# Optimization experiments

Hardware: AMD Instinct MI355X
Metric: run time of the kernel (lower is better)

## Reference

```python
import jax, jax.numpy as jnp
import numpy as np


def _bilinear_resize(x, out_h, out_w):
    """PyTorch F.interpolate(mode='bilinear', align_corners=False) on NCHW."""
    H, W = x.shape[-2], x.shape[-1]

    def coords(out, inp):
        scale = inp / out
        src = (jnp.arange(out, dtype=jnp.float32) + 0.5) * scale - 0.5
        src = jnp.clip(src, 0.0, inp - 1)
        lo = jnp.floor(src).astype(jnp.int32)
        hi = jnp.minimum(lo + 1, inp - 1)
        w = src - lo.astype(jnp.float32)
        return lo, hi, w

    yl, yh, wy = coords(out_h, H)
    xl, xh, wx = coords(out_w, W)
    rows = x[..., yl, :] * (1.0 - wy)[:, None] + x[..., yh, :] * wy[:, None]  # (B,F,out_h,W)
    out = rows[..., xl] * (1.0 - wx) + rows[..., xh] * wx  # (B,F,out_h,out_w)
    return out


def setup_inputs() -> dict:
    key = jax.random.key(0)
    x = jax.random.normal(key, (32, 3, 256, 256), dtype=jnp.float32)
    return {"x": x}


def reference(x):
    B, C, H, W = x.shape
    feats = []
    for p in (2, 4, 8):
        stride = p // 2
        n = (H - p) // stride + 1  # square input -> nh == nw == n
        starts = jnp.arange(n) * stride
        off = jnp.arange(p)
        idx = starts[:, None] + off[None, :]  # (n, p)
        # gather overlapping windows: (B,C,n,p,W) -> (B,C,n,p,n,p)
        xp = x[:, :, idx, :]
        xp = xp[:, :, :, :, idx]
        # -> (B,C,n,n,p,p) row-major patch flatten, matching torch unfold
        xp = xp.transpose(0, 1, 2, 4, 3, 5).reshape(B, C, n * n, p * p)
        mean = xp.mean(-1)                               # (B,C,N)
        std = jnp.std(xp, axis=-1, ddof=1) + 1e-6        # unbiased, like torch.std
        if p == 2:
            a, b, c, d = xp[..., 0], xp[..., 1], xp[..., 2], xp[..., 3]
            raw = a * d - b * c                          # det of 2x2 patch
            det = jnp.sign(raw) * jnp.abs(raw) ** 0.7
            det = det.mean(axis=1, keepdims=True)        # (B,1,N)
            comb = jnp.concatenate([mean, std, det], axis=1)
        else:
            comb = jnp.concatenate([mean, std], axis=1)
        spatial = comb.reshape(B, -1, n, n)
        feats.append(_bilinear_resize(spatial, 32, 32))
    return jnp.concatenate(feats, axis=1)  # (B, 19, 32, 32) for C=3
```

## Files before the change

### kernel.cpp

```cpp
#include <hip/hip_runtime.h>
#include <math.h>


__device__ __forceinline__ float hsum4(float4 q) { return q.x + q.y + q.z + q.w; }
__device__ __forceinline__ float hsq4(float4 q) {
    return q.x * q.x + q.y * q.y + q.z * q.z + q.w * q.w;
}

__device__ __forceinline__ float signed_pow07(float raw) {
    float a = fabsf(raw);
    float r = exp2f(0.7f * log2f(fmaxf(a, 1e-38f)));
    return copysignf(r, raw);
}

template <int N>
__device__ __forceinline__ void bilin(int o, int& lo, float& w) {
    const float scale = (float)N / 32.0f;
    float s = (o + 0.5f) * scale - 0.5f;
    s = fminf(fmaxf(s, 0.0f), (float)(N - 1));
    lo = (int)floorf(s);
    w = s - (float)lo;
}

__device__ __forceinline__ void spds_scale8(const float* __restrict__ x,
                                            float* __restrict__ out, int tid) {
    constexpr int N = 63;
    constexpr float INV_PP = 1.0f / 64.0f, INV_PPM1 = 1.0f / 63.0f;

    int lane_y = tid & 1;
    int t      = tid >> 1;
    int ox     = t & 31;
    int oy     = (t >> 5) & 31;
    int u      = t >> 10;
    int b      = u / 3;
    int c      = u - 3 * b;

    int yl, xl; float wy, wx;
    bilin<N>(oy, yl, wy);
    bilin<N>(ox, xl, wx);

    float wly = lane_y ? wy : (1.0f - wy);
    float wl  = (1.0f - wx) * wly;
    float wr  = wx * wly;

    const float* xc = x + ((size_t)b * 3 + c) * 65536 + xl * 4;

    int rb    = yl * 4 + (lane_y ? 11 : 0);
    int rstep = lane_y ? -256 : 256;
    const float* p = xc + rb * 256;
    float Xs_l = 0, Xs_r = 0, Xq_l = 0, Xq_r = 0;
    float Ys_l = 0, Ys_r = 0, Yq_l = 0, Yq_r = 0;
    #pragma unroll
    for (int dy = 0; dy < 6; ++dy) {
        const float4* r = reinterpret_cast<const float4*>(p);
        float4 q0 = r[0], q1 = r[1], q2 = r[2];
        float s0 = hsum4(q0), s1 = hsum4(q1), s2 = hsum4(q2);
        float t0 = hsq4(q0),  t1 = hsq4(q1),  t2 = hsq4(q2);
        float srl = s0 + s1, srr = s1 + s2;
        float trl = t0 + t1, trr = t1 + t2;
        Xs_l += srl; Xs_r += srr; Xq_l += trl; Xq_r += trr;
        if (dy < 4) { Ys_l += srl; Ys_r += srr; Yq_l += trl; Yq_r += trr; }
        p += rstep;
    }
    float Zs_l = Xs_l - Ys_l, Zs_r = Xs_r - Ys_r;
    float Zq_l = Xq_l - Yq_l, Zq_r = Xq_r - Yq_r;
    float sl  = Xs_l + __shfl_xor(Zs_l, 1);
    float sr  = Xs_r + __shfl_xor(Zs_r, 1);
    float ssl = Xq_l + __shfl_xor(Zq_l, 1);
    float ssr = Xq_r + __shfl_xor(Zq_r, 1);

    float ml = sl * INV_PP, mr = sr * INV_PP;
    float vl = (ssl - sl * sl * INV_PP) * INV_PPM1;
    float vr = (ssr - sr * sr * INV_PP) * INV_PPM1;
    float dl = sqrtf(fmaxf(vl, 0.0f)) + 1e-6f;
    float dr = sqrtf(fmaxf(vr, 0.0f)) + 1e-6f;

    float vmean = ml * wl + mr * wr;
    float vstd  = dl * wl + dr * wr;
    vmean += __shfl_xor(vmean, 1);
    vstd  += __shfl_xor(vstd, 1);

    if (lane_y == 0) {
        float* ob = out + ((size_t)b * 19 + 13 + c) * 1024 + oy * 32 + ox;
        ob[0]        = vmean;
        ob[3 * 1024] = vstd;
    }
}

template <int P, int CHBASE>
__device__ __forceinline__ void spds_scale(const float* __restrict__ x,
                                           float* __restrict__ out, int tid) {
    constexpr int N = (256 - P) / (P / 2) + 1;
    constexpr int NV = (P == 2) ? 7 : 6;
    constexpr int PP = P * P;
    constexpr float INV_PP   = 1.0f / PP;
    constexpr float INV_PPM1 = 1.0f / (PP - 1);

    int lane_y = tid & 1;
    int t      = tid >> 1;
    int ox     = t & 31;
    int oy     = (t >> 5) & 31;
    int b      = t >> 10;

    int yl, xl; float wy, wx;
    bilin<N>(oy, yl, wy);
    bilin<N>(ox, xl, wx);

    float wly = lane_y ? wy : (1.0f - wy);
    float wl  = (1.0f - wx) * wly;
    float wr  = wx * wly;

    const float* xb = x + (size_t)b * 3 * 65536 + xl * (P / 2);

    float vals[7];
    float det = 0.0f;

    #pragma unroll
    for (int c = 0; c < 3; ++c) {
        const float* xc = xb + (size_t)c * 65536;
        float sl, ssl, sr, ssr;
        float rawl = 0.0f, rawr = 0.0f;

        if constexpr (P == 4) {
            int rb    = yl * 2 + (lane_y ? 5 : 0);
            int rstep = lane_y ? -256 : 256;
            const float* p = xc + rb * 256;
            float Xs_l = 0, Xs_r = 0, Xq_l = 0, Xq_r = 0;
            float Ys_l = 0, Ys_r = 0, Yq_l = 0, Yq_r = 0;
            #pragma unroll
            for (int dy = 0; dy < 3; ++dy) {
                const float2* r = reinterpret_cast<const float2*>(p);
                float2 u = r[0], v = r[1], w2 = r[2];
                float s0 = u.x + u.y, s1 = v.x + v.y, s2 = w2.x + w2.y;
                float t0 = u.x * u.x + u.y * u.y;
                float t1 = v.x * v.x + v.y * v.y;
                float t2 = w2.x * w2.x + w2.y * w2.y;
                float srl = s0 + s1, srr = s1 + s2;
                float trl = t0 + t1, trr = t1 + t2;
                Xs_l += srl; Xs_r += srr; Xq_l += trl; Xq_r += trr;
                if (dy < 2) { Ys_l += srl; Ys_r += srr; Yq_l += trl; Yq_r += trr; }
                p += rstep;
            }
            float Zs_l = Xs_l - Ys_l, Zs_r = Xs_r - Ys_r;
            float Zq_l = Xq_l - Yq_l, Zq_r = Xq_r - Yq_r;
            sl  = Xs_l + __shfl_xor(Zs_l, 1);
            sr  = Xs_r + __shfl_xor(Zs_r, 1);
            ssl = Xq_l + __shfl_xor(Zq_l, 1);
            ssr = Xq_r + __shfl_xor(Zq_r, 1);
        } else {
            const float* p0 = xc + (yl + lane_y) * 256;
            float a  = p0[0],   b2 = p0[1],   e = p0[2];
            float c2 = p0[256], d  = p0[257], g = p0[258];
            sl  = a + b2 + c2 + d;
            sr  = b2 + e + d + g;
            ssl = a * a + b2 * b2 + c2 * c2 + d * d;
            ssr = b2 * b2 + e * e + d * d + g * g;
            rawl = a * d - b2 * c2;
            rawr = b2 * g - e * d;
        }

        float ml = sl * INV_PP, mr = sr * INV_PP;
        float vl = (ssl - sl * sl * INV_PP) * INV_PPM1;
        float vr = (ssr - sr * sr * INV_PP) * INV_PPM1;
        float dl = sqrtf(fmaxf(vl, 0.0f)) + 1e-6f;
        float dr = sqrtf(fmaxf(vr, 0.0f)) + 1e-6f;

        vals[c]     = ml * wl + mr * wr;
        vals[3 + c] = dl * wl + dr * wr;
        if constexpr (P == 2)
            det += signed_pow07(rawl) * wl + signed_pow07(rawr) * wr;
    }
    if constexpr (P == 2) vals[6] = det * (1.0f / 3.0f);

    #pragma unroll
    for (int i = 0; i < NV; ++i) {
        float v = vals[i];
        v += __shfl_xor(v, 1);
        vals[i] = v;
    }

    if (lane_y == 0) {
        float* ob = out + ((size_t)b * 19 + CHBASE) * 1024 + oy * 32 + ox;
        #pragma unroll
        for (int i = 0; i < NV; ++i)
            ob[(size_t)i * 1024] = vals[i];
    }
}

__global__ __launch_bounds__(256) void spds_fused(const float* __restrict__ x,
                                                  float* __restrict__ out,
                                                  int bps8, int bps) {
    int bid = blockIdx.x;
    if (bid < bps8) {
        spds_scale8(x, out, bid * 256 + threadIdx.x);
    } else if (bid < bps8 + bps) {
        spds_scale<4, 7>(x, out, (bid - bps8) * 256 + threadIdx.x);
    } else {
        spds_scale<2, 0>(x, out, (bid - bps8 - bps) * 256 + threadIdx.x);
    }
}

extern "C" void kernel_launch(void* const* d_in, const int* in_sizes, int n_in,
                              void* d_out, int out_size, void* d_ws, size_t ws_size,
                              hipStream_t stream) {
    const float* x   = (const float*)d_in[0];
    float*       out = (float*)d_out;
    int B = in_sizes[0] / (3 * 256 * 256);
    int bps8 = B * 24;
    int bps  = B * 8;
    spds_fused<<<bps8 + 2 * bps, 256, 0, stream>>>(x, out, bps8, bps);
}
```

Measured before the change: 11.13 us.

## Stage 8x8 patch statistics through shared-memory 2x2 and 4x4 block sums

Replaces the per-thread scale-8 path, which reread overlapping 8x8 windows straight from global memory, with a block-cooperative scheme. Each block loads a 68-row band of one channel once, builds 2x2 sum and sum-of-squares partials in LDS, reduces them to 4x4 partials, and assembles each needed 8x8 window from four 4x4 tiles. This halves the scale-8 block count and cuts redundant global reads. In exchange it adds about 43KB of static shared memory to every block of the fused kernel, including the scale-2 and scale-4 blocks that never use it, which may limit occupancy.

Result: slower. 12.73 us (+14.4%).

```diff
diff --git a/kernel.cpp b/kernel.cpp
--- a/kernel.cpp
+++ b/kernel.cpp
@@ -20,71 +20,6 @@
     s = fminf(fmaxf(s, 0.0f), (float)(N - 1));
     lo = (int)floorf(s);
     w = s - (float)lo;
-}
-
-__device__ __forceinline__ void spds_scale8(const float* __restrict__ x,
-                                            float* __restrict__ out, int tid) {
-    constexpr int N = 63;
-    constexpr float INV_PP = 1.0f / 64.0f, INV_PPM1 = 1.0f / 63.0f;
-
-    int lane_y = tid & 1;
-    int t      = tid >> 1;
-    int ox     = t & 31;
-    int oy     = (t >> 5) & 31;
-    int u      = t >> 10;
-    int b      = u / 3;
-    int c      = u - 3 * b;
-
-    int yl, xl; float wy, wx;
-    bilin<N>(oy, yl, wy);
-    bilin<N>(ox, xl, wx);
-
-    float wly = lane_y ? wy : (1.0f - wy);
-    float wl  = (1.0f - wx) * wly;
-    float wr  = wx * wly;
-
-    const float* xc = x + ((size_t)b * 3 + c) * 65536 + xl * 4;
-
-    int rb    = yl * 4 + (lane_y ? 11 : 0);
-    int rstep = lane_y ? -256 : 256;
-    const float* p = xc + rb * 256;
-    float Xs_l = 0, Xs_r = 0, Xq_l = 0, Xq_r = 0;
-    float Ys_l = 0, Ys_r = 0, Yq_l = 0, Yq_r = 0;
-    #pragma unroll
-    for (int dy = 0; dy < 6; ++dy) {
-        const float4* r = reinterpret_cast<const float4*>(p);
-        float4 q0 = r[0], q1 = r[1], q2 = r[2];
-        float s0 = hsum4(q0), s1 = hsum4(q1), s2 = hsum4(q2);
-        float t0 = hsq4(q0),  t1 = hsq4(q1),  t2 = hsq4(q2);
-        float srl = s0 + s1, srr = s1 + s2;
-        float trl = t0 + t1, trr = t1 + t2;
-        Xs_l += srl; Xs_r += srr; Xq_l += trl; Xq_r += trr;
-        if (dy < 4) { Ys_l += srl; Ys_r += srr; Yq_l += trl; Yq_r += trr; }
-        p += rstep;
-    }
-    float Zs_l = Xs_l - Ys_l, Zs_r = Xs_r - Ys_r;
-    float Zq_l = Xq_l - Yq_l, Zq_r = Xq_r - Yq_r;
-    float sl  = Xs_l + __shfl_xor(Zs_l, 1);
-    float sr  = Xs_r + __shfl_xor(Zs_r, 1);
-    float ssl = Xq_l + __shfl_xor(Zq_l, 1);
-    float ssr = Xq_r + __shfl_xor(Zq_r, 1);
-
-    float ml = sl * INV_PP, mr = sr * INV_PP;
-    float vl = (ssl - sl * sl * INV_PP) * INV_PPM1;
-    float vr = (ssr - sr * sr * INV_PP) * INV_PPM1;
-    float dl = sqrtf(fmaxf(vl, 0.0f)) + 1e-6f;
-    float dr = sqrtf(fmaxf(vr, 0.0f)) + 1e-6f;
-
-    float vmean = ml * wl + mr * wr;
-    float vstd  = dl * wl + dr * wr;
-    vmean += __shfl_xor(vmean, 1);
-    vstd  += __shfl_xor(vstd, 1);
-
-    if (lane_y == 0) {
-        float* ob = out + ((size_t)b * 19 + 13 + c) * 1024 + oy * 32 + ox;
-        ob[0]        = vmean;
-        ob[3 * 1024] = vstd;
-    }
 }
 
 template <int P, int CHBASE>
@@ -189,14 +124,105 @@
 
 __global__ __launch_bounds__(256) void spds_fused(const float* __restrict__ x,
                                                   float* __restrict__ out,
-                                                  int bps8, int bps) {
+                                                  int nb8, int bps) {
+    __shared__ float2 B22[34 * 128];
+    __shared__ float2 B44[17 * 64];
+
     int bid = blockIdx.x;
-    if (bid < bps8) {
-        spds_scale8(x, out, bid * 256 + threadIdx.x);
-    } else if (bid < bps8 + bps) {
-        spds_scale<4, 7>(x, out, (bid - bps8) * 256 + threadIdx.x);
+    if (bid < nb8) {
+        int rem = bid % 12;
+        int b   = bid / 12;
+        int c   = rem >> 2;
+        int t   = rem & 3;
+        const int R0q_tab[4] = {0, 16, 31, 47};
+        int R0q = R0q_tab[t];
+        int R0  = R0q * 4;
+
+        const float* xc = x + ((size_t)b * 3 + c) * 65536;
+
+        #pragma unroll
+        for (int k = 0; k < 9; ++k) {
+            int tau = threadIdx.x + 256 * k;
+            if (tau < 34 * 64) {
+                int q = tau & 63;
+                int r2 = tau >> 6;
+                const float* p = xc + (R0 + 2 * r2) * 256 + 4 * q;
+                float4 a  = *reinterpret_cast<const float4*>(p);
+                float4 b4 = *reinterpret_cast<const float4*>(p + 256);
+                float s0  = a.x + a.y + b4.x + b4.y;
+                float ss0 = a.x * a.x + a.y * a.y + b4.x * b4.x + b4.y * b4.y;
+                float s1  = a.z + a.w + b4.z + b4.w;
+                float ss1 = a.z * a.z + a.w * a.w + b4.z * b4.z + b4.w * b4.w;
+                B22[2 * tau]     = make_float2(s0, ss0);
+                B22[2 * tau + 1] = make_float2(s1, ss1);
+            }
+        }
+        __syncthreads();
+
+        #pragma unroll
+        for (int k = 0; k < 5; ++k) {
+            int tau = threadIdx.x + 256 * k;
+            if (tau < 17 * 64) {
+                int c4 = tau & 63;
+                int r4 = tau >> 6;
+                int i0 = (2 * r4) * 128 + 2 * c4;
+                float2 p00 = B22[i0],       p01 = B22[i0 + 1];
+                float2 p10 = B22[i0 + 128], p11 = B22[i0 + 129];
+                B44[tau] = make_float2(p00.x + p01.x + p10.x + p11.x,
+                                       p00.y + p01.y + p10.y + p11.y);
+            }
+        }
+        __syncthreads();
+
+        constexpr float INV_PP = 1.0f / 64.0f, INV_PPM1 = 1.0f / 63.0f;
+        #pragma unroll
+        for (int k = 0; k < 2; ++k) {
+            int tau = threadIdx.x + 256 * k;
+            int ly  = tau & 1;
+            int pix = tau >> 1;
+            int ox  = pix & 31;
+            int oy  = t * 8 + (pix >> 5);
+
+            int yl, xl; float wy, wx;
+            bilin<63>(oy, yl, wy);
+            bilin<63>(ox, xl, wx);
+
+            float wly = ly ? wy : (1.0f - wy);
+            float wl  = (1.0f - wx) * wly;
+            float wr  = wx * wly;
+
+            int rr = yl + ly - R0q;
+            const float2* r0 = &B44[rr * 64 + xl];
+            const float2* r1 = r0 + 64;
+            float2 c00 = r0[0], c01 = r0[1], c02 = r0[2];
+            float2 c10 = r1[0], c11 = r1[1], c12 = r1[2];
+
+            float sl  = c00.x + c01.x + c10.x + c11.x;
+            float ssl = c00.y + c01.y + c10.y + c11.y;
+            float sr  = c01.x + c02.x + c11.x + c12.x;
+            float ssr = c01.y + c02.y + c11.y + c12.y;
+
+            float ml = sl * INV_PP, mr = sr * INV_PP;
+            float vlv = (ssl - sl * sl * INV_PP) * INV_PPM1;
+            float vrv = (ssr - sr * sr * INV_PP) * INV_PPM1;
+            float dl = sqrtf(fmaxf(vlv, 0.0f)) + 1e-6f;
+            float dr = sqrtf(fmaxf(vrv, 0.0f)) + 1e-6f;
+
+            float vmean = ml * wl + mr * wr;
+            float vstd  = dl * wl + dr * wr;
+            vmean += __shfl_xor(vmean, 1);
+            vstd  += __shfl_xor(vstd, 1);
+
+            if (ly == 0) {
+                float* ob = out + ((size_t)b * 19 + 13 + c) * 1024 + oy * 32 + ox;
+                ob[0]        = vmean;
+                ob[3 * 1024] = vstd;
+            }
+        }
+    } else if (bid < nb8 + bps) {
+        spds_scale<4, 7>(x, out, (bid - nb8) * 256 + threadIdx.x);
     } else {
-        spds_scale<2, 0>(x, out, (bid - bps8 - bps) * 256 + threadIdx.x);
+        spds_scale<2, 0>(x, out, (bid - nb8 - bps) * 256 + threadIdx.x);
     }
 }
 
@@ -206,7 +232,7 @@
     const float* x   = (const float*)d_in[0];
     float*       out = (float*)d_out;
     int B = in_sizes[0] / (3 * 256 * 256);
-    int bps8 = B * 24;
-    int bps  = B * 8;
-    spds_fused<<<bps8 + 2 * bps, 256, 0, stream>>>(x, out, bps8, bps);
-}
+    int nb8 = B * 12;
+    int bps = B * 8;
+    spds_fused<<<nb8 + 2 * bps, 256, 0, stream>>>(x, out, nb8, bps);
+}
```
